# Performance work log

Hardware: AMD Instinct MI355X
Metric: run time of the kernel (lower is better)

The kernel has to match this reference:

```python
import jax, jax.numpy as jnp
import numpy as np

N_HEAD = 16  # matches init_kwargs


def _rope_cos_sin(T, head_dim):
    # inv_freq over even indices, as in AdvancedRotaryEmbedding
    inv_freq = 1.0 / (10000.0 ** (jnp.arange(0, head_dim, 2, dtype=jnp.float32) / head_dim))
    t = jnp.arange(T, dtype=jnp.float32)
    freqs = t[:, None] * inv_freq[None, :]  # [T, head_dim/2]
    return jnp.cos(freqs), jnp.sin(freqs)


def _apply_rope(x, cos, sin):
    # x: [B, H, T, D]; cos/sin: [T, D/2] (broadcast over B, H)
    x1, x2 = x[..., 0::2], x[..., 1::2]
    # half-concat layout, faithful to the module's apply_rotary_emb
    return jnp.concatenate([x1 * cos - x2 * sin, x1 * sin + x2 * cos], axis=-1)


def reference(x, Wq, Wk, Wv, Wo):
    B, T, C = x.shape
    H = N_HEAD
    D = C // H
    # QKV projections (torch Linear: y = x @ W.T), then split heads -> [B, H, T, D]
    q = (x @ Wq.T).reshape(B, T, H, D).transpose(0, 2, 1, 3)
    k = (x @ Wk.T).reshape(B, T, H, D).transpose(0, 2, 1, 3)
    v = (x @ Wv.T).reshape(B, T, H, D).transpose(0, 2, 1, 3)
    cos, sin = _rope_cos_sin(T, D)
    cos = cos.astype(x.dtype)
    sin = sin.astype(x.dtype)
    q = _apply_rope(q, cos, sin)
    k = _apply_rope(k, cos, sin)
    # causal SDPA (eval mode -> dropout_p = 0); jax.nn expects [B, T, H, D]
    y = jax.nn.dot_product_attention(
        q.transpose(0, 2, 1, 3),
        k.transpose(0, 2, 1, 3),
        v.transpose(0, 2, 1, 3),
        is_causal=True,
    )  # [B, T, H, D]
    y = y.reshape(B, T, C)
    return y @ Wo.T


def setup_inputs() -> dict:
    key = jax.random.key(0)
    ks = jax.random.split(key, 5)
    B, T, C = 2, 2048, 1024
    s = 1.0 / np.sqrt(C)
    return {
        "x": jax.random.normal(ks[0], (B, T, C), dtype=jnp.float32),
        "Wq": jax.random.normal(ks[1], (C, C), dtype=jnp.float32) * s,
        "Wk": jax.random.normal(ks[2], (C, C), dtype=jnp.float32) * s,
        "Wv": jax.random.normal(ks[3], (C, C), dtype=jnp.float32) * s,
        "Wo": jax.random.normal(ks[4], (C, C), dtype=jnp.float32) * s,
    }
```

## Files before the change

kernel.cpp:

```cpp
#include <hip/hip_runtime.h>
#include <cstdint>
#include <cstddef>

typedef short s16x8 __attribute__((ext_vector_type(8)));
typedef float f32x4 __attribute__((ext_vector_type(4)));

#define MFMA16(a, b, c) __builtin_amdgcn_mfma_f32_16x16x32_bf16((a), (b), (c), 0, 0, 0)

constexpr int LDP = 72;
constexpr int LDW = 136;

__device__ __forceinline__ short f2bf(float f) {
    unsigned u = __builtin_bit_cast(unsigned, f);
    u += 0x7FFFu + ((u >> 16) & 1u);
    return (short)(u >> 16);
}
__device__ __forceinline__ float bf2f(short s) {
    unsigned u = ((unsigned)(unsigned short)s) << 16;
    return __builtin_bit_cast(float, u);
}
__device__ __forceinline__ unsigned pack2(float a, float b) {
    return (unsigned)(unsigned short)f2bf(a) | ((unsigned)(unsigned short)f2bf(b) << 16);
}
__device__ __forceinline__ unsigned pack2t(float a, float b) {
    unsigned ua = __builtin_bit_cast(unsigned, a);
    unsigned ub = __builtin_bit_cast(unsigned, b);
    return (ua >> 16) | (ub & 0xFFFF0000u);
}

__device__ __forceinline__ void async_ld16(const void* g, void* l) {
    __builtin_amdgcn_global_load_lds(
        (const __attribute__((address_space(1))) unsigned int*)g,
        (__attribute__((address_space(3))) unsigned int*)l, 16, 0, 0);
}

__global__ __launch_bounds__(256) void convert_kernel(
    const float* __restrict__ x, const float* __restrict__ Wq,
    const float* __restrict__ Wk, const float* __restrict__ Wv,
    const float* __restrict__ Wo, short* __restrict__ xb, short* __restrict__ wb) {
    const size_t f = ((size_t)blockIdx.x * 256 + threadIdx.x) * 8;
    const float* src;
    short* dst;
    if (f < 4194304) { src = x + f; dst = xb + f; }
    else {
        size_t wo = f - 4194304;
        int seg = (int)(wo >> 20);
        const float* ws4[4] = {Wq, Wk, Wv, Wo};
        src = ws4[seg] + (wo & 1048575u);
        dst = wb + wo;
    }
    float4 a = ((const float4*)src)[0];
    float4 b = ((const float4*)src)[1];
    *(uint4*)dst = make_uint4(pack2(a.x, a.y), pack2(a.z, a.w),
                              pack2(b.x, b.y), pack2(b.z, b.w));
}

__global__ __launch_bounds__(256) void qkv_kernel(
    const short* __restrict__ xb, const short* __restrict__ wb,
    short* __restrict__ Qo, short* __restrict__ Ko, short* __restrict__ VTo) {
    __shared__ __align__(16) short sA[128 * 64];
    __shared__ __align__(16) short sB[128 * 64];
    const int tid = threadIdx.x;
    const int w = tid >> 6, lane = tid & 63, quad = lane >> 4, l15 = lane & 15;
    const int wm = w & 1, wn = w >> 1;
    const int bx = blockIdx.x, by = blockIdx.y;
    const int m0 = by * 128;
    const int nb = bx * 128;

    f32x4 acc[4][4];
#pragma unroll
    for (int i = 0; i < 4; i++)
#pragma unroll
        for (int j = 0; j < 4; j++) acc[i][j] = f32x4{0.f, 0.f, 0.f, 0.f};

    for (int kb = 0; kb < 16; kb++) {
        const int k0 = kb * 64;
        if (kb) __syncthreads();
#pragma unroll
        for (int i = 0; i < 4; i++) {
            int c = i * 256 + tid;
            int row = c >> 3, col8 = (c & 7) * 8;
            async_ld16(xb + (size_t)(m0 + row) * 1024 + k0 + col8,
                       &sA[(i * 256 + w * 64) * 8]);
            async_ld16(wb + (size_t)(nb + row) * 1024 + k0 + col8,
                       &sB[(i * 256 + w * 64) * 8]);
        }
        __syncthreads();
#pragma unroll
        for (int ks = 0; ks < 2; ks++) {
            s16x8 av[4], bv[4];
#pragma unroll
            for (int at = 0; at < 4; at++)
                av[at] = *(const s16x8*)&sA[(wm * 64 + at * 16 + l15) * 64 + ks * 32 + quad * 8];
#pragma unroll
            for (int bt = 0; bt < 4; bt++)
                bv[bt] = *(const s16x8*)&sB[(wn * 64 + bt * 16 + l15) * 64 + ks * 32 + quad * 8];
#pragma unroll
            for (int at = 0; at < 4; at++)
#pragma unroll
                for (int bt = 0; bt < 4; bt++)
                    acc[at][bt] = MFMA16(av[at], bv[bt], acc[at][bt]);
        }
    }

    const int wsel = bx >> 3;
    const int h = (bx & 7) * 2 + wn;
    if (wsel == 2) {
#pragma unroll
        for (int at = 0; at < 4; at++) {
            int m = m0 + wm * 64 + at * 16 + quad * 4;
            int b = m >> 11, t0 = m & 2047;
            size_t base = ((size_t)((b * 16 + h) * 64)) * 2048;
#pragma unroll
            for (int bt = 0; bt < 4; bt++) {
                int d = bt * 16 + l15;
                unsigned lo = pack2(acc[at][bt][0], acc[at][bt][1]);
                unsigned hi = pack2(acc[at][bt][2], acc[at][bt][3]);
                *(uint2*)&VTo[base + (size_t)d * 2048 + t0] = make_uint2(lo, hi);
            }
        }
    } else {
        short* Out = (wsel == 0) ? Qo : Ko;
#pragma unroll
        for (int at = 0; at < 4; at++)
#pragma unroll
            for (int r = 0; r < 4; r++) {
                int m = m0 + wm * 64 + at * 16 + quad * 4 + r;
                int b = m >> 11, t = m & 2047;
                size_t base = (((size_t)(b * 16 + h)) * 2048 + t) * 64;
#pragma unroll
                for (int bt = 0; bt < 4; bt++)
                    Out[base + bt * 16 + l15] = f2bf(acc[at][bt][r]);
            }
    }
}

__global__ __launch_bounds__(256) void rope_kernel(short* __restrict__ Q, short* __restrict__ K) {
    const int rid = blockIdx.x * 256 + threadIdx.x;
    const bool isK = (rid & 65536) != 0;
    short* buf = isK ? K : Q;
    const float sc = isK ? 1.0f : 0.18033688011112042f;
    const int r2 = rid & 65535;
    const int t = r2 & 2047;
    short* row = buf + (size_t)r2 * 64;

    unsigned wv[32];
    const uint4* rp = (const uint4*)row;
#pragma unroll
    for (int c = 0; c < 8; c++) {
        uint4 v = rp[c];
        wv[c * 4 + 0] = v.x; wv[c * 4 + 1] = v.y; wv[c * 4 + 2] = v.z; wv[c * 4 + 3] = v.w;
    }
    float y1[32], y2[32];
    const float tf = (float)t;
#pragma unroll
    for (int i = 0; i < 32; i++) {
        float x1 = bf2f((short)(wv[i] & 0xFFFFu));
        float x2 = bf2f((short)(wv[i] >> 16));
        float inv = exp2f((float)i * -0.4152410118609203f);
        float rev = tf * inv * 0.15915494309189535f;
        rev = rev - floorf(rev);
        float sn = __builtin_amdgcn_sinf(rev);
        float cs = __builtin_amdgcn_cosf(rev);
        y1[i] = (x1 * cs - x2 * sn) * sc;
        y2[i] = (x1 * sn + x2 * cs) * sc;
    }
    unsigned ow[32];
#pragma unroll
    for (int i = 0; i < 16; i++) ow[i] = pack2(y1[2 * i], y1[2 * i + 1]);
#pragma unroll
    for (int i = 0; i < 16; i++) ow[16 + i] = pack2(y2[2 * i], y2[2 * i + 1]);
    uint4* wp = (uint4*)row;
#pragma unroll
    for (int c = 0; c < 8; c++)
        wp[c] = make_uint4(ow[c * 4 + 0], ow[c * 4 + 1], ow[c * 4 + 2], ow[c * 4 + 3]);
}

__global__ __launch_bounds__(256) void attn_kernel(
    const short* __restrict__ Q, const short* __restrict__ K,
    const short* __restrict__ VT, short* __restrict__ paO, float* __restrict__ ml) {
    __shared__ __align__(16) short sQP[64 * LDW];
    __shared__ __align__(16) short sK[128 * LDP];
    __shared__ __align__(16) short sVT[64 * LDW];

    const int tid = threadIdx.x;
    const int w = tid >> 6, lane = tid & 63, quad = lane >> 4, l15 = lane & 15;
    const int u = 79 - blockIdx.x;
    const int bh = blockIdx.y;

    int qt, c;
    if (u < 8)       { qt = u; c = 0; }
    else if (u < 24) { int v = u - 8;  qt = 8 + (v >> 1); c = v & 1; }
    else if (u < 48) { int v = u - 24; qt = 16 + v / 3;   c = v - 3 * (qt - 16); }
    else             { int v = u - 48; qt = 24 + (v >> 2); c = v & 3; }
    const int kbDiag = qt >> 1;
    const int kb0 = c * 4;
    const int kb1 = min(kb0 + 3, kbDiag);

    const short* Qp = Q + (size_t)bh * 2048 * 64;
    const short* Kp = K + (size_t)bh * 2048 * 64;
    const short* Vp = VT + (size_t)bh * 64 * 2048;

#pragma unroll
    for (int i = 0; i < 2; i++) {
        int p = tid + i * 256;
        int row = p >> 3, c8 = p & 7;
        uint4 v = *(const uint4*)(Qp + (size_t)(qt * 64 + row) * 64 + c8 * 8);
        *(uint4*)&sQP[row * LDW + c8 * 8] = v;
    }
    __syncthreads();
    s16x8 aq[2];
#pragma unroll
    for (int ks = 0; ks < 2; ks++)
        aq[ks] = *(const s16x8*)&sQP[(w * 16 + l15) * LDW + ks * 32 + quad * 8];

    f32x4 o[4];
#pragma unroll
    for (int i = 0; i < 4; i++) o[i] = f32x4{0.f, 0.f, 0.f, 0.f};
    float lrun = 0.f;
    const int q_idx = qt * 64 + w * 16 + l15;

    for (int kb = kb0; kb <= kb1; kb++) {
        __syncthreads();
#pragma unroll
        for (int i = 0; i < 4; i++) {
            int p = tid + i * 256;
            {
                int row = p >> 3, c8 = p & 7;
                uint4 kv = *(const uint4*)(Kp + (size_t)(kb * 128 + row) * 64 + c8 * 8);
                *(uint4*)&sK[row * LDP + c8 * 8] = kv;
            }
            {
                int row = p >> 4, c16 = p & 15;
                uint4 vv = *(const uint4*)(Vp + (size_t)row * 2048 + kb * 128 + c16 * 8);
                *(uint4*)&sVT[row * LDW + c16 * 8] = vv;
            }
        }
        __syncthreads();

        f32x4 sa[8];
#pragma unroll
        for (int i = 0; i < 8; i++) sa[i] = f32x4{0.f, 0.f, 0.f, 0.f};
#pragma unroll
        for (int ks = 0; ks < 2; ks++) {
#pragma unroll
            for (int ct = 0; ct < 8; ct++) {
                s16x8 kf = *(const s16x8*)&sK[(ct * 16 + l15) * LDP + ks * 32 + quad * 8];
                sa[ct] = MFMA16(kf, aq[ks], sa[ct]);
            }
        }

        float ps[8][4];
#pragma unroll
        for (int ct = 0; ct < 8; ct++)
#pragma unroll
            for (int r = 0; r < 4; r++) ps[ct][r] = sa[ct][r];

        if (kb == kbDiag) {
#pragma unroll
            for (int ct = 0; ct < 8; ct++) {
                int kbase = kb * 128 + ct * 16 + quad * 4;
#pragma unroll
                for (int r = 0; r < 4; r++)
                    if ((kbase + r) > q_idx) ps[ct][r] = -INFINITY;
            }
        }

        float cm[8];
#pragma unroll
        for (int ct = 0; ct < 8; ct++) {
#pragma unroll
            for (int r = 0; r < 4; r++) ps[ct][r] = exp2f(ps[ct][r]);
            cm[ct] = (ps[ct][0] + ps[ct][1]) + (ps[ct][2] + ps[ct][3]);
        }
        lrun += ((cm[0] + cm[1]) + (cm[2] + cm[3])) + ((cm[4] + cm[5]) + (cm[6] + cm[7]));

#pragma unroll
        for (int ct = 0; ct < 8; ct++) {
            unsigned lo = pack2t(ps[ct][0], ps[ct][1]);
            unsigned hi = pack2t(ps[ct][2], ps[ct][3]);
            *(uint2*)&sQP[(w * 16 + l15) * LDW + ct * 16 + quad * 4] = make_uint2(lo, hi);
        }

#pragma unroll
        for (int ks2 = 0; ks2 < 4; ks2++) {
            s16x8 pa = *(const s16x8*)&sQP[(w * 16 + l15) * LDW + ks2 * 32 + quad * 8];
#pragma unroll
            for (int ct = 0; ct < 4; ct++) {
                s16x8 vb = *(const s16x8*)&sVT[(ct * 16 + l15) * LDW + ks2 * 32 + quad * 8];
                o[ct] = MFMA16(pa, vb, o[ct]);
            }
        }
    }

    const size_t pbase = ((size_t)(bh * 80 + u)) * 4096;
#pragma unroll
    for (int r = 0; r < 4; r++) {
        int row = w * 16 + quad * 4 + r;
#pragma unroll
        for (int ct = 0; ct < 4; ct++)
            paO[pbase + row * 64 + ct * 16 + l15] = f2bf(o[ct][r]);
    }
    lrun += __shfl_xor(lrun, 16);
    lrun += __shfl_xor(lrun, 32);
    if (quad == 0)
        ml[(bh * 80 + u) * 64 + w * 16 + l15] = lrun;
}

__global__ __launch_bounds__(256) void combine_kernel(
    const short* __restrict__ paO, const float* __restrict__ ml, short* __restrict__ Y) {
    const int qt = blockIdx.x, bh = blockIdx.y;
    const int b = bh >> 4, h = bh & 15;
    const int nch = (qt >> 3) + 1;
    int base;
    if (qt < 8) base = qt;
    else if (qt < 16) base = 8 + 2 * (qt - 8);
    else if (qt < 24) base = 24 + 3 * (qt - 16);
    else base = 48 + 4 * (qt - 24);

    const int row = threadIdx.x >> 2;
    const int cq = (threadIdx.x & 3) * 16;

    float L = 0.f;
    for (int i = 0; i < nch; i++)
        L += ml[(bh * 80 + base + i) * 64 + row];
    const float inv = 1.0f / L;

    float acc[16];
#pragma unroll
    for (int j = 0; j < 16; j++) acc[j] = 0.f;
    for (int i = 0; i < nch; i++) {
        const short* p = paO + ((size_t)(bh * 80 + base + i)) * 4096 + row * 64 + cq;
        uint4 v0 = ((const uint4*)p)[0];
        uint4 v1 = ((const uint4*)p)[1];
        unsigned vs[8] = {v0.x, v0.y, v0.z, v0.w, v1.x, v1.y, v1.z, v1.w};
#pragma unroll
        for (int j = 0; j < 8; j++) {
            acc[2 * j + 0] += bf2f((short)(vs[j] & 0xFFFFu));
            acc[2 * j + 1] += bf2f((short)(vs[j] >> 16));
        }
    }
    const int t = qt * 64 + row;
    short* yp = Y + ((size_t)(b * 2048 + t)) * 1024 + h * 64 + cq;
    unsigned ow[8];
#pragma unroll
    for (int j = 0; j < 8; j++) ow[j] = pack2(acc[2 * j] * inv, acc[2 * j + 1] * inv);
    ((uint4*)yp)[0] = make_uint4(ow[0], ow[1], ow[2], ow[3]);
    ((uint4*)yp)[1] = make_uint4(ow[4], ow[5], ow[6], ow[7]);
}

__global__ __launch_bounds__(256) void oproj_kernel(
    const short* __restrict__ Yb, const short* __restrict__ Wob, float* __restrict__ out) {
    __shared__ __align__(16) short sA[64 * 64];
    __shared__ __align__(16) short sB[128 * 64];
    const int tid = threadIdx.x;
    const int w = tid >> 6, lane = tid & 63, quad = lane >> 4, l15 = lane & 15;
    const int m0 = blockIdx.y * 64;
    const int nb = blockIdx.x * 128;

    f32x4 acc[4][2];
#pragma unroll
    for (int i = 0; i < 4; i++)
#pragma unroll
        for (int j = 0; j < 2; j++) acc[i][j] = f32x4{0.f, 0.f, 0.f, 0.f};

    for (int kb = 0; kb < 16; kb++) {
        const int k0 = kb * 64;
        if (kb) __syncthreads();
#pragma unroll
        for (int i = 0; i < 2; i++) {
            int c = i * 256 + tid;
            int row = c >> 3, col8 = (c & 7) * 8;
            async_ld16(Yb + (size_t)(m0 + row) * 1024 + k0 + col8,
                       &sA[(i * 256 + w * 64) * 8]);
        }
#pragma unroll
        for (int i = 0; i < 4; i++) {
            int c = i * 256 + tid;
            int row = c >> 3, col8 = (c & 7) * 8;
            async_ld16(Wob + (size_t)(nb + row) * 1024 + k0 + col8,
                       &sB[(i * 256 + w * 64) * 8]);
        }
        __syncthreads();
#pragma unroll
        for (int ks = 0; ks < 2; ks++) {
            s16x8 av[4], bv[2];
#pragma unroll
            for (int at = 0; at < 4; at++)
                av[at] = *(const s16x8*)&sA[(at * 16 + l15) * 64 + ks * 32 + quad * 8];
#pragma unroll
            for (int bt = 0; bt < 2; bt++)
                bv[bt] = *(const s16x8*)&sB[(w * 32 + bt * 16 + l15) * 64 + ks * 32 + quad * 8];
#pragma unroll
            for (int at = 0; at < 4; at++)
#pragma unroll
                for (int bt = 0; bt < 2; bt++)
                    acc[at][bt] = MFMA16(av[at], bv[bt], acc[at][bt]);
        }
    }
#pragma unroll
    for (int at = 0; at < 4; at++)
#pragma unroll
        for (int r = 0; r < 4; r++) {
            int m = m0 + at * 16 + quad * 4 + r;
#pragma unroll
            for (int bt = 0; bt < 2; bt++) {
                int n = nb + w * 32 + bt * 16 + l15;
                out[(size_t)m * 1024 + n] = acc[at][bt][r];
            }
        }
}

extern "C" void kernel_launch(void* const* d_in, const int* in_sizes, int n_in,
                              void* d_out, int out_size, void* d_ws, size_t ws_size,
                              hipStream_t stream) {
    (void)in_sizes; (void)n_in; (void)out_size; (void)ws_size;
    const float* x  = (const float*)d_in[0];
    const float* Wq = (const float*)d_in[1];
    const float* Wk = (const float*)d_in[2];
    const float* Wv = (const float*)d_in[3];
    const float* Wo = (const float*)d_in[4];
    float* out = (float*)d_out;

    const size_t NE = (size_t)2 * 16 * 2048 * 64;
    short* Q   = (short*)d_ws;
    short* K   = Q + NE;
    short* VT  = K + NE;
    short* Y   = VT + NE;
    short* xb  = Y;
    short* wb  = Y + NE;
    short* paO = wb + NE;
    float* ml  = (float*)(paO + (size_t)32 * 80 * 4096);

    convert_kernel<<<4096, 256, 0, stream>>>(x, Wq, Wk, Wv, Wo, xb, wb);
    qkv_kernel<<<dim3(24, 32), 256, 0, stream>>>(xb, wb, Q, K, VT);
    rope_kernel<<<512, 256, 0, stream>>>(Q, K);
    attn_kernel<<<dim3(80, 32), 256, 0, stream>>>(Q, K, VT, paO, ml);
    combine_kernel<<<dim3(32, 32), 256, 0, stream>>>(paO, ml, Y);
    oproj_kernel<<<dim3(8, 64), 256, 0, stream>>>(Y, wb + 3 * 1048576, out);
}
```

Baseline: 204.3 us.

## Prefetch next K/V tile into registers during attention compute

Global loads of the next K and V tile now go into registers right after the shared-memory barrier, so their latency overlaps with the QK and PV MFMA work of the current tile. The Q load is also issued together with the first K/V load. It additionally raises wave priority around the MFMA loops and uses the raw hardware exp2 intrinsic in place of exp2f. The cost is more register pressure from holding eight uint4 prefetch registers, which could lower occupancy.

```diff
diff --git a/kernel.cpp b/kernel.cpp
--- a/kernel.cpp
+++ b/kernel.cpp
@@ -201,12 +201,27 @@
     const short* Kp = K + (size_t)bh * 2048 * 64;
     const short* Vp = VT + (size_t)bh * 64 * 2048;
 
+    uint4 kreg[4], vreg[4];
+    auto LOADKV = [&](int kb) {
+#pragma unroll
+        for (int i = 0; i < 4; i++) {
+            int p = tid + i * 256;
+            kreg[i] = *(const uint4*)(Kp + (size_t)(kb * 128 + (p >> 3)) * 64 + (p & 7) * 8);
+            vreg[i] = *(const uint4*)(Vp + (size_t)(p >> 4) * 2048 + kb * 128 + (p & 15) * 8);
+        }
+    };
+
+    uint4 qv[2];
 #pragma unroll
     for (int i = 0; i < 2; i++) {
         int p = tid + i * 256;
-        int row = p >> 3, c8 = p & 7;
-        uint4 v = *(const uint4*)(Qp + (size_t)(qt * 64 + row) * 64 + c8 * 8);
-        *(uint4*)&sQP[row * LDW + c8 * 8] = v;
+        qv[i] = *(const uint4*)(Qp + (size_t)(qt * 64 + (p >> 3)) * 64 + (p & 7) * 8);
+    }
+    LOADKV(kb0);
+#pragma unroll
+    for (int i = 0; i < 2; i++) {
+        int p = tid + i * 256;
+        *(uint4*)&sQP[(p >> 3) * LDW + (p & 7) * 8] = qv[i];
     }
     __syncthreads();
     s16x8 aq[2];
@@ -225,22 +240,16 @@
 #pragma unroll
         for (int i = 0; i < 4; i++) {
             int p = tid + i * 256;
-            {
-                int row = p >> 3, c8 = p & 7;
-                uint4 kv = *(const uint4*)(Kp + (size_t)(kb * 128 + row) * 64 + c8 * 8);
-                *(uint4*)&sK[row * LDP + c8 * 8] = kv;
-            }
-            {
-                int row = p >> 4, c16 = p & 15;
-                uint4 vv = *(const uint4*)(Vp + (size_t)row * 2048 + kb * 128 + c16 * 8);
-                *(uint4*)&sVT[row * LDW + c16 * 8] = vv;
-            }
+            *(uint4*)&sK[(p >> 3) * LDP + (p & 7) * 8] = kreg[i];
+            *(uint4*)&sVT[(p >> 4) * LDW + (p & 15) * 8] = vreg[i];
         }
         __syncthreads();
+        if (kb < kb1) LOADKV(kb + 1);
 
         f32x4 sa[8];
 #pragma unroll
         for (int i = 0; i < 8; i++) sa[i] = f32x4{0.f, 0.f, 0.f, 0.f};
+        __builtin_amdgcn_s_setprio(1);
 #pragma unroll
         for (int ks = 0; ks < 2; ks++) {
 #pragma unroll
@@ -249,6 +258,7 @@
                 sa[ct] = MFMA16(kf, aq[ks], sa[ct]);
             }
         }
+        __builtin_amdgcn_s_setprio(0);
 
         float ps[8][4];
 #pragma unroll
@@ -270,7 +280,7 @@
 #pragma unroll
         for (int ct = 0; ct < 8; ct++) {
 #pragma unroll
-            for (int r = 0; r < 4; r++) ps[ct][r] = exp2f(ps[ct][r]);
+            for (int r = 0; r < 4; r++) ps[ct][r] = __builtin_amdgcn_exp2f(ps[ct][r]);
             cm[ct] = (ps[ct][0] + ps[ct][1]) + (ps[ct][2] + ps[ct][3]);
         }
         lrun += ((cm[0] + cm[1]) + (cm[2] + cm[3])) + ((cm[4] + cm[5]) + (cm[6] + cm[7]));
@@ -282,6 +292,7 @@
             *(uint2*)&sQP[(w * 16 + l15) * LDW + ct * 16 + quad * 4] = make_uint2(lo, hi);
         }
 
+        __builtin_amdgcn_s_setprio(1);
 #pragma unroll
         for (int ks2 = 0; ks2 < 4; ks2++) {
             s16x8 pa = *(const s16x8*)&sQP[(w * 16 + l15) * LDW + ks2 * 32 + quad * 8];
@@ -291,6 +302,7 @@
                 o[ct] = MFMA16(pa, vb, o[ct]);
             }
         }
+        __builtin_amdgcn_s_setprio(0);
     }
 
     const size_t pbase = ((size_t)(bh * 80 + u)) * 4096;
```

After: 260.2 us. 1.27x slower.
